# Optimization experiments

Hardware: AMD Instinct MI355X
Metric: run time of the kernel (lower is better)

Reference implementation:

```python
import jax, jax.numpy as jnp
from jax import lax
import numpy as np

INPUT_SIZE = 128
T = 64
B = 8192
HIDDENS = [32, 16, 8]
FUTURE = 1


def _lstm_layer(x, w_ih, w_hh, b_ih, b_hh):
    """PyTorch-semantics single-layer LSTM, batch_first, zero init state.
    x: [B,T,D]; w_ih: [4H,D]; w_hh: [4H,H]; b_ih,b_hh: [4H]. Gate order i,f,g,o.
    Returns all hidden states [B,T,H]."""
    Bsz = x.shape[0]
    H = w_hh.shape[1]
    # Precompute input contribution for all timesteps in one big GEMM.
    xg = jnp.einsum('btd,gd->btg', x, w_ih) + b_ih + b_hh  # [B,T,4H]
    xg_t = jnp.swapaxes(xg, 0, 1)  # [T,B,4H]

    def step(carry, xt):
        h, c = carry
        gates = xt + h @ w_hh.T  # [B,4H]
        i, f, g, o = jnp.split(gates, 4, axis=-1)
        i = jax.nn.sigmoid(i)
        f = jax.nn.sigmoid(f)
        g = jnp.tanh(g)
        o = jax.nn.sigmoid(o)
        c = f * c + i * g
        h = o * jnp.tanh(c)
        return (h, c), h

    init = (jnp.zeros((Bsz, H), x.dtype), jnp.zeros((Bsz, H), x.dtype))
    _, hs = lax.scan(step, init, xg_t)  # hs: [T,B,H]
    return jnp.swapaxes(hs, 0, 1)


def setup_inputs() -> dict:
    key = jax.random.key(0)
    ks = jax.random.split(key, 16)
    s = 0.1

    def rn(k, shape):
        return jax.random.normal(k, shape, dtype=jnp.float32) * s

    inp = {
        'x': jax.random.normal(ks[0], (B, T, INPUT_SIZE), dtype=jnp.float32),
        'w_ih1': rn(ks[1], (4 * 32, INPUT_SIZE)),
        'w_hh1': rn(ks[2], (4 * 32, 32)),
        'b_ih1': rn(ks[3], (4 * 32,)),
        'b_hh1': rn(ks[4], (4 * 32,)),
        'w_ih2': rn(ks[5], (4 * 16, 32)),
        'w_hh2': rn(ks[6], (4 * 16, 16)),
        'b_ih2': rn(ks[7], (4 * 16,)),
        'b_hh2': rn(ks[8], (4 * 16,)),
        'w_ih3': rn(ks[9], (4 * 8, 16)),
        'w_hh3': rn(ks[10], (4 * 8, 8)),
        'b_ih3': rn(ks[11], (4 * 8,)),
        'b_hh3': rn(ks[12], (4 * 8,)),
        'fc_w': rn(ks[13], (FUTURE, 8)),
        'fc_b': rn(ks[14], (FUTURE,)),
    }
    return inp


def reference(x, w_ih1, w_hh1, b_ih1, b_hh1, w_ih2, w_hh2, b_ih2, b_hh2,
              w_ih3, w_hh3, b_ih3, b_hh3, fc_w, fc_b):
    h = _lstm_layer(x, w_ih1, w_hh1, b_ih1, b_hh1)   # [B,T,32]
    h = _lstm_layer(h, w_ih2, w_hh2, b_ih2, b_hh2)   # [B,T,16]
    h = _lstm_layer(h, w_ih3, w_hh3, b_ih3, b_hh3)   # [B,T,8]
    return h[:, -1, :] @ fc_w.T + fc_b               # [B, FUTURE]
```

## Files before the change

### kernel.cpp

```cpp
#include <hip/hip_runtime.h>
#include <cstddef>
#include <type_traits>


typedef _Float16 h8_t  __attribute__((ext_vector_type(8)));
typedef __fp16   p2_t  __attribute__((ext_vector_type(2)));
typedef float    f4_t  __attribute__((ext_vector_type(4)));

#define T_LEN 64
#define D_IN  128

__device__ __forceinline__ float rcp_(float x) { return __builtin_amdgcn_rcpf(x); }

__device__ __forceinline__ float cell_(float vi, float vf, float vg, float vo,
                                       float& c) {
    float eni = __expf(-vi);
    float enf = __expf(-vf);
    float eno = __expf(-vo);
    float e2g = __expf(2.0f * vg);
    float igg = (e2g - 1.0f) * rcp_((1.0f + eni) * (e2g + 1.0f));
    c = rcp_(1.0f + enf) * c + igg;
    float t2 = fminf(fmaxf(2.0f * c, -30.0f), 30.0f);
    float e2c = __expf(t2);
    return (e2c - 1.0f) * rcp_((1.0f + eno) * (e2c + 1.0f));
}

__device__ __forceinline__ h8_t zero8h() {
    h8_t r = { (_Float16)0.f,(_Float16)0.f,(_Float16)0.f,(_Float16)0.f,
               (_Float16)0.f,(_Float16)0.f,(_Float16)0.f,(_Float16)0.f };
    return r;
}
__device__ __forceinline__ h8_t cvt8(f4_t lo, f4_t hi) {
    union { h8_t v8; p2_t v2[4]; } u;
    u.v2[0] = __builtin_amdgcn_cvt_pkrtz(lo[0], lo[1]);
    u.v2[1] = __builtin_amdgcn_cvt_pkrtz(lo[2], lo[3]);
    u.v2[2] = __builtin_amdgcn_cvt_pkrtz(hi[0], hi[1]);
    u.v2[3] = __builtin_amdgcn_cvt_pkrtz(hi[2], hi[3]);
    return u.v8;
}
__device__ __forceinline__ h8_t load8f_h(const float* __restrict__ p) {
    f4_t lo = *(const f4_t*)p, hi = *(const f4_t*)(p + 4);
    return cvt8(lo, hi);
}

__device__ __forceinline__ void bar_lds() {
    asm volatile("s_waitcnt lgkmcnt(0)" ::: "memory");
    __builtin_amdgcn_s_barrier();
}

__global__ __launch_bounds__(256, 2)
void lstm_one(const float* __restrict__ x,
              const float* __restrict__ w_ih1, const float* __restrict__ w_hh1,
              const float* __restrict__ b_ih1, const float* __restrict__ b_hh1,
              const float* __restrict__ w_ih2, const float* __restrict__ w_hh2,
              const float* __restrict__ b_ih2, const float* __restrict__ b_hh2,
              const float* __restrict__ w_ih3, const float* __restrict__ w_hh3,
              const float* __restrict__ b_ih3, const float* __restrict__ b_hh3,
              const float* __restrict__ fc_w, const float* __restrict__ fc_b,
              float* __restrict__ out)
{
    __shared__ __align__(16) _Float16 h1s[2][16][40];
    __shared__ __align__(16) _Float16 h2s[2][16][24];
    __shared__ __align__(16) _Float16 h3s[2][16][8];
    __shared__ __align__(16) _Float16 xs[2][16 * 128];

    const int tid  = threadIdx.x;
    const int lane = tid & 63;
    const int wid  = tid >> 6;
    const int nl = lane & 15, qd = lane >> 4;
    const int n7 = nl & 7;
    const bool lo8 = (nl & 8) == 0;

    h8_t bw1[2][4], bh1[2];
    #pragma unroll
    for (int j = 0; j < 2; ++j) {
        int G = 8 * wid + n7 + 32 * ((nl >> 3) + 2 * j);
        #pragma unroll
        for (int kc = 0; kc < 4; ++kc)
            bw1[j][kc] = load8f_h(w_ih1 + G * 128 + kc * 32 + qd * 8);
        bh1[j] = load8f_h(w_hh1 + G * 32 + qd * 8);
    }
    h8_t bw2[2] = {zero8h(), zero8h()}, bh2[2] = {zero8h(), zero8h()};
    float bs2[4] = {0.f, 0.f, 0.f, 0.f};
    if (wid < 2) {
        #pragma unroll
        for (int j = 0; j < 2; ++j) {
            int G = 32 * j + 16 * (nl >> 3) + 8 * wid + n7;
            bw2[j] = load8f_h(w_ih2 + G * 32 + qd * 8);
            bh2[j] = (qd < 2) ? load8f_h(w_hh2 + G * 16 + qd * 8) : zero8h();
        }
        int u2 = 8 * wid + n7;
        #pragma unroll
        for (int g = 0; g < 4; ++g) bs2[g] = b_ih2[16 * g + u2] + b_hh2[16 * g + u2];
    }
    h8_t b3c[2] = {zero8h(), zero8h()};
    float bs3[4] = {0.f, 0.f, 0.f, 0.f};
    if (wid >= 2) {
        #pragma unroll
        for (int j = 0; j < 2; ++j) {
            int G = 16 * j + 8 * (nl >> 3) + n7;
            b3c[j] = (qd < 2) ? load8f_h(w_ih3 + G * 16 + qd * 8)
                   : (qd == 2) ? load8f_h(w_hh3 + G * 8) : zero8h();
        }
        #pragma unroll
        for (int g = 0; g < 4; ++g) bs3[g] = b_ih3[8 * g + n7] + b_hh3[8 * g + n7];
    }
    float bs1[4];
    {
        int u1 = 8 * wid + n7;
        #pragma unroll
        for (int g = 0; g < 4; ++g) bs1[g] = b_ih1[32 * g + u1] + b_hh1[32 * g + u1];
    }

    for (int i = tid; i < 2 * 16 * 40; i += 256) (&h1s[0][0][0])[i] = (_Float16)0.f;
    for (int i = tid; i < 2 * 16 * 24; i += 256) (&h2s[0][0][0])[i] = (_Float16)0.f;
    for (int i = tid; i < 2 * 16 * 8;  i += 256) (&h3s[0][0][0])[i] = (_Float16)0.f;

    float c1[2] = {0.f, 0.f};
    float c2[2] = {0.f, 0.f};
    float c3    = 0.f;

    const int b0 = blockIdx.x * 16;

    const int xrow = tid >> 4, xcc = tid & 15;
    const float* xg = x + ((size_t)(b0 + xrow) * T_LEN) * D_IN + xcc * 8;
    const int xws = (xrow * 16 + (xcc ^ (xrow & 7))) * 8;

    f4_t xa0 = *(const f4_t*)xg, xa1 = *(const f4_t*)(xg + 4);
    *(h8_t*)&xs[0][xws] = cvt8(xa0, xa1);
    xa0 = *(const f4_t*)(xg + D_IN);
    xa1 = *(const f4_t*)(xg + D_IN + 4);
    bar_lds();

    auto step = [&](auto d1c, auto d2c, auto d3c, auto pc, int t) {
        constexpr bool DO1 = decltype(d1c)::value;
        constexpr bool DO2 = decltype(d2c)::value;
        constexpr bool DO3 = decltype(d3c)::value;
        constexpr int  P   = decltype(pc)::value;

        h8_t a1p = zero8h();
        if constexpr (DO1 || DO2)
            a1p = *(const h8_t*)&h1s[1 - P][nl][qd * 8];

        if constexpr (DO1) {
            h8_t af[4];
            #pragma unroll
            for (int kc = 0; kc < 4; ++kc)
                af[kc] = *(const h8_t*)&xs[P][(nl * 16 + ((4 * kc + qd) ^ n7)) * 8];

            h8_t xcur = cvt8(xa0, xa1);
            {
                int tn = (t + 2 < T_LEN) ? (t + 2) : (T_LEN - 1);
                const float* xn = xg + (size_t)tn * D_IN;
                xa0 = *(const f4_t*)xn;
                xa1 = *(const f4_t*)(xn + 4);
            }
            *(h8_t*)&xs[1 - P][xws] = xcur;

            f4_t acc[2];
            #pragma unroll
            for (int j = 0; j < 2; ++j) {
                f4_t a_ = {0.f, 0.f, 0.f, 0.f};
                #pragma unroll
                for (int kc = 0; kc < 4; ++kc)
                    a_ = __builtin_amdgcn_mfma_f32_16x16x32_f16(af[kc], bw1[j][kc], a_, 0, 0, 0);
                a_ = __builtin_amdgcn_mfma_f32_16x16x32_f16(a1p, bh1[j], a_, 0, 0, 0);
                acc[j] = a_;
            }
            #pragma unroll
            for (int rr = 0; rr < 2; ++rr) {
                float s0 = lo8 ? acc[0][rr + 2] : acc[0][rr];
                float s1 = lo8 ? acc[1][rr + 2] : acc[1][rr];
                float x0 = __shfl_xor(s0, 8, 64);
                float x1 = __shfl_xor(s1, 8, 64);
                float vi = lo8 ? acc[0][rr] : x0;
                float vf = lo8 ? x0 : acc[0][rr + 2];
                float vg = lo8 ? acc[1][rr] : x1;
                float vo = lo8 ? x1 : acc[1][rr + 2];
                float h = cell_(vi + bs1[0], vf + bs1[1], vg + bs1[2], vo + bs1[3], c1[rr]);
                h1s[P][4 * qd + rr + (lo8 ? 0 : 2)][8 * wid + n7] = (_Float16)h;
            }
        }

        if constexpr (DO2) {
            if (wid < 2) {
                h8_t a2p = zero8h();
                if (qd < 2) a2p = *(const h8_t*)&h2s[P][nl][qd * 8];
                f4_t acc2[2];
                #pragma unroll
                for (int j = 0; j < 2; ++j) {
                    f4_t a_ = {0.f, 0.f, 0.f, 0.f};
                    a_ = __builtin_amdgcn_mfma_f32_16x16x32_f16(a1p, bw2[j], a_, 0, 0, 0);
                    a_ = __builtin_amdgcn_mfma_f32_16x16x32_f16(a2p, bh2[j], a_, 0, 0, 0);
                    acc2[j] = a_;
                }
                #pragma unroll
                for (int rr = 0; rr < 2; ++rr) {
                    float s0 = lo8 ? acc2[0][rr + 2] : acc2[0][rr];
                    float s1 = lo8 ? acc2[1][rr + 2] : acc2[1][rr];
                    float x0 = __shfl_xor(s0, 8, 64);
                    float x1 = __shfl_xor(s1, 8, 64);
                    float vi = lo8 ? acc2[0][rr] : x0;
                    float vf = lo8 ? x0 : acc2[0][rr + 2];
                    float vg = lo8 ? acc2[1][rr] : x1;
                    float vo = lo8 ? x1 : acc2[1][rr + 2];
                    float h = cell_(vi + bs2[0], vf + bs2[1], vg + bs2[2], vo + bs2[3], c2[rr]);
                    h2s[1 - P][4 * qd + rr + (lo8 ? 0 : 2)][8 * wid + n7] = (_Float16)h;
                }
            }
        }

        if constexpr (DO3) {
            if (wid >= 2) {
                h8_t a3 = zero8h();
                if (qd < 2)       a3 = *(const h8_t*)&h2s[P][nl][qd * 8];
                else if (qd == 2) a3 = *(const h8_t*)&h3s[1 - P][nl][0];
                f4_t acc3[2];
                #pragma unroll
                for (int j = 0; j < 2; ++j) {
                    f4_t a_ = {0.f, 0.f, 0.f, 0.f};
                    acc3[j] = __builtin_amdgcn_mfma_f32_16x16x32_f16(a3, b3c[j], a_, 0, 0, 0);
                }
                auto l3c = [&](auto rpc) {
                    constexpr int rp = decltype(rpc)::value;
                    float eLo = acc3[0][rp],     oLo = acc3[1][rp];
                    float eHi = acc3[0][rp + 2], oHi = acc3[1][rp + 2];
                    float se = lo8 ? eHi : eLo; float xe = __shfl_xor(se, 8, 64);
                    float so = lo8 ? oHi : oLo; float xo = __shfl_xor(so, 8, 64);
                    float vi = lo8 ? eLo : xe;
                    float vf = lo8 ? xe  : eHi;
                    float vg = lo8 ? oLo : xo;
                    float vo = lo8 ? xo  : oHi;
                    float h = cell_(vi + bs3[0], vf + bs3[1], vg + bs3[2], vo + bs3[3], c3);
                    h3s[P][4 * qd + rp + (lo8 ? 0 : 2)][n7] = (_Float16)h;
                };
                if (wid == 2) l3c(std::integral_constant<int, 0>{});
                else          l3c(std::integral_constant<int, 1>{});
            }
        }

        bar_lds();
    };

    using TT = std::integral_constant<bool, true>;
    using FF = std::integral_constant<bool, false>;
    using P0 = std::integral_constant<int, 0>;
    using P1 = std::integral_constant<int, 1>;

    step(TT{}, FF{}, FF{}, P0{}, 0);
    step(TT{}, TT{}, FF{}, P1{}, 1);
    for (int tb = 1; tb < 32; ++tb) {
        step(TT{}, TT{}, TT{}, P0{}, 2 * tb);
        step(TT{}, TT{}, TT{}, P1{}, 2 * tb + 1);
    }
    step(FF{}, TT{}, TT{}, P0{}, 64);
    step(FF{}, FF{}, TT{}, P1{}, 65);

    if (tid < 16) {
        float a = fc_b[0];
        #pragma unroll
        for (int u = 0; u < 8; ++u)
            a += fc_w[u] * (float)h3s[1][tid][u];
        out[b0 + tid] = a;
    }
}

extern "C" void kernel_launch(void* const* d_in, const int* in_sizes, int n_in,
                              void* d_out, int out_size, void* d_ws, size_t ws_size,
                              hipStream_t stream) {
    (void)in_sizes; (void)n_in; (void)out_size; (void)d_ws; (void)ws_size;
    const float* x     = (const float*)d_in[0];
    const float* w_ih1 = (const float*)d_in[1];
    const float* w_hh1 = (const float*)d_in[2];
    const float* b_ih1 = (const float*)d_in[3];
    const float* b_hh1 = (const float*)d_in[4];
    const float* w_ih2 = (const float*)d_in[5];
    const float* w_hh2 = (const float*)d_in[6];
    const float* b_ih2 = (const float*)d_in[7];
    const float* b_hh2 = (const float*)d_in[8];
    const float* w_ih3 = (const float*)d_in[9];
    const float* w_hh3 = (const float*)d_in[10];
    const float* b_ih3 = (const float*)d_in[11];
    const float* b_hh3 = (const float*)d_in[12];
    const float* fc_w  = (const float*)d_in[13];
    const float* fc_b  = (const float*)d_in[14];

    dim3 grid(512), block(256);
    hipLaunchKernelGGL(lstm_one, grid, block, 0, stream,
                       x, w_ih1, w_hh1, b_ih1, b_hh1,
                       w_ih2, w_hh2, b_ih2, b_hh2,
                       w_ih3, w_hh3, b_ih3, b_hh3,
                       fc_w, fc_b, (float*)d_out);
}
```

Measured before the change: 391.0 us.

## Load x directly into MFMA fragment registers and split MFMA accumulation chains

Drops the shared-memory staging buffer for x. Each lane now loads its own 32 fp32 input values per timestep straight into registers in MFMA A-fragment layout, prefetching one step ahead instead of two. This removes the LDS write and swizzled reads for x, though each wave now loads the full 16x128 tile redundantly instead of sharing one load across the block. The dependent MFMA chains are also split into independent partial accumulators that are summed with vector adds, which shortens the dependency latency on the serial recurrence path.

```diff
diff --git a/kernel.cpp b/kernel.cpp
--- a/kernel.cpp
+++ b/kernel.cpp
@@ -62,7 +62,6 @@
     __shared__ __align__(16) _Float16 h1s[2][16][40];
     __shared__ __align__(16) _Float16 h2s[2][16][24];
     __shared__ __align__(16) _Float16 h3s[2][16][8];
-    __shared__ __align__(16) _Float16 xs[2][16 * 128];
 
     const int tid  = threadIdx.x;
     const int lane = tid & 63;
@@ -122,14 +121,13 @@
 
     const int b0 = blockIdx.x * 16;
 
-    const int xrow = tid >> 4, xcc = tid & 15;
-    const float* xg = x + ((size_t)(b0 + xrow) * T_LEN) * D_IN + xcc * 8;
-    const int xws = (xrow * 16 + (xcc ^ (xrow & 7))) * 8;
-
-    f4_t xa0 = *(const f4_t*)xg, xa1 = *(const f4_t*)(xg + 4);
-    *(h8_t*)&xs[0][xws] = cvt8(xa0, xa1);
-    xa0 = *(const f4_t*)(xg + D_IN);
-    xa1 = *(const f4_t*)(xg + D_IN + 4);
+    const float* xgl = x + ((size_t)(b0 + nl) * T_LEN) * D_IN + qd * 8;
+    f4_t xr[8];
+    #pragma unroll
+    for (int kc = 0; kc < 4; ++kc) {
+        xr[2 * kc]     = *(const f4_t*)(xgl + kc * 32);
+        xr[2 * kc + 1] = *(const f4_t*)(xgl + kc * 32 + 4);
+    }
     bar_lds();
 
     auto step = [&](auto d1c, auto d2c, auto d3c, auto pc, int t) {
@@ -145,27 +143,27 @@
         if constexpr (DO1) {
             h8_t af[4];
             #pragma unroll
-            for (int kc = 0; kc < 4; ++kc)
-                af[kc] = *(const h8_t*)&xs[P][(nl * 16 + ((4 * kc + qd) ^ n7)) * 8];
-
-            h8_t xcur = cvt8(xa0, xa1);
+            for (int kc = 0; kc < 4; ++kc) af[kc] = cvt8(xr[2 * kc], xr[2 * kc + 1]);
             {
-                int tn = (t + 2 < T_LEN) ? (t + 2) : (T_LEN - 1);
-                const float* xn = xg + (size_t)tn * D_IN;
-                xa0 = *(const f4_t*)xn;
-                xa1 = *(const f4_t*)(xn + 4);
-            }
-            *(h8_t*)&xs[1 - P][xws] = xcur;
+                int tn = (t + 1 < T_LEN) ? (t + 1) : t;
+                const float* xn = xgl + (size_t)tn * D_IN;
+                #pragma unroll
+                for (int kc = 0; kc < 4; ++kc) {
+                    xr[2 * kc]     = *(const f4_t*)(xn + kc * 32);
+                    xr[2 * kc + 1] = *(const f4_t*)(xn + kc * 32 + 4);
+                }
+            }
 
             f4_t acc[2];
             #pragma unroll
             for (int j = 0; j < 2; ++j) {
-                f4_t a_ = {0.f, 0.f, 0.f, 0.f};
-                #pragma unroll
-                for (int kc = 0; kc < 4; ++kc)
-                    a_ = __builtin_amdgcn_mfma_f32_16x16x32_f16(af[kc], bw1[j][kc], a_, 0, 0, 0);
-                a_ = __builtin_amdgcn_mfma_f32_16x16x32_f16(a1p, bh1[j], a_, 0, 0, 0);
-                acc[j] = a_;
+                f4_t z = {0.f, 0.f, 0.f, 0.f};
+                f4_t ax = __builtin_amdgcn_mfma_f32_16x16x32_f16(af[0], bw1[j][0], z, 0, 0, 0);
+                ax = __builtin_amdgcn_mfma_f32_16x16x32_f16(af[1], bw1[j][1], ax, 0, 0, 0);
+                f4_t ay = __builtin_amdgcn_mfma_f32_16x16x32_f16(af[2], bw1[j][2], z, 0, 0, 0);
+                ay = __builtin_amdgcn_mfma_f32_16x16x32_f16(af[3], bw1[j][3], ay, 0, 0, 0);
+                f4_t ah = __builtin_amdgcn_mfma_f32_16x16x32_f16(a1p, bh1[j], z, 0, 0, 0);
+                acc[j] = (ax + ay) + ah;
             }
             #pragma unroll
             for (int rr = 0; rr < 2; ++rr) {
@@ -189,10 +187,10 @@
                 f4_t acc2[2];
                 #pragma unroll
                 for (int j = 0; j < 2; ++j) {
-                    f4_t a_ = {0.f, 0.f, 0.f, 0.f};
-                    a_ = __builtin_amdgcn_mfma_f32_16x16x32_f16(a1p, bw2[j], a_, 0, 0, 0);
-                    a_ = __builtin_amdgcn_mfma_f32_16x16x32_f16(a2p, bh2[j], a_, 0, 0, 0);
-                    acc2[j] = a_;
+                    f4_t z = {0.f, 0.f, 0.f, 0.f};
+                    f4_t m1 = __builtin_amdgcn_mfma_f32_16x16x32_f16(a1p, bw2[j], z, 0, 0, 0);
+                    f4_t m2 = __builtin_amdgcn_mfma_f32_16x16x32_f16(a2p, bh2[j], z, 0, 0, 0);
+                    acc2[j] = m1 + m2;
                 }
                 #pragma unroll
                 for (int rr = 0; rr < 2; ++rr) {
@@ -218,8 +216,8 @@
                 f4_t acc3[2];
                 #pragma unroll
                 for (int j = 0; j < 2; ++j) {
-                    f4_t a_ = {0.f, 0.f, 0.f, 0.f};
-                    acc3[j] = __builtin_amdgcn_mfma_f32_16x16x32_f16(a3, b3c[j], a_, 0, 0, 0);
+                    f4_t z = {0.f, 0.f, 0.f, 0.f};
+                    acc3[j] = __builtin_amdgcn_mfma_f32_16x16x32_f16(a3, b3c[j], z, 0, 0, 0);
                 }
                 auto l3c = [&](auto rpc) {
                     constexpr int rp = decltype(rpc)::value;
```

Result: slower. 418.0 us (+6.9%).

## Make each wave own four batch rows independently, removing block barriers per step

Applied to the files above, without the earlier changes.

Reassigns work so each wavefront processes its own 4 batch rows through all three LSTM layers, instead of four waves cooperating on 16 rows with per-step block barriers. The per-step s_barrier is removed because all cross-step state is wave-private, and layer-2/3 and recurrent layer-1 weights move to a shared LDS pool. The cost is that MFMA tiles now use only 4 of 16 rows, so matrix work per useful row grows about fourfold. Each wave also runs every layer's cell math, and the extra weight registers and LDS reads add pressure.

```diff
diff --git a/kernel.cpp b/kernel.cpp
--- a/kernel.cpp
+++ b/kernel.cpp
@@ -9,6 +9,7 @@
 
 #define T_LEN 64
 #define D_IN  128
+#define XS_STR 132
 
 __device__ __forceinline__ float rcp_(float x) { return __builtin_amdgcn_rcpf(x); }
 
@@ -43,11 +44,6 @@
     return cvt8(lo, hi);
 }
 
-__device__ __forceinline__ void bar_lds() {
-    asm volatile("s_waitcnt lgkmcnt(0)" ::: "memory");
-    __builtin_amdgcn_s_barrier();
-}
-
 __global__ __launch_bounds__(256, 2)
 void lstm_one(const float* __restrict__ x,
               const float* __restrict__ w_ih1, const float* __restrict__ w_hh1,
@@ -59,78 +55,100 @@
               const float* __restrict__ fc_w, const float* __restrict__ fc_b,
               float* __restrict__ out)
 {
-    __shared__ __align__(16) _Float16 h1s[2][16][40];
-    __shared__ __align__(16) _Float16 h2s[2][16][24];
-    __shared__ __align__(16) _Float16 h3s[2][16][8];
-    __shared__ __align__(16) _Float16 xs[2][16 * 128];
+    __shared__ __align__(16) _Float16 h1s[4][2][4][40];
+    __shared__ __align__(16) _Float16 h2s[4][2][4][24];
+    __shared__ __align__(16) _Float16 h3s[4][2][4][8];
+    __shared__ __align__(16) _Float16 xs [4][2][4][XS_STR];
+    __shared__ __align__(16) _Float16 wpool[18][64][8];
+    __shared__ __align__(16) _Float16 zpad[8];
 
     const int tid  = threadIdx.x;
     const int lane = tid & 63;
     const int wid  = tid >> 6;
     const int nl = lane & 15, qd = lane >> 4;
     const int n7 = nl & 7;
-    const bool lo8 = (nl & 8) == 0;
-
-    h8_t bw1[2][4], bh1[2];
+    const int hi8 = (nl >> 3) & 1;
+    const bool lo8 = hi8 == 0;
+    const int row4 = nl & 3;
+    const bool q1 = (qd & 1) != 0, q2 = (qd & 2) != 0;
+
+    auto RS = [&](f4_t a) -> float {
+        float t01 = q1 ? a[1] : a[0];
+        float t23 = q1 ? a[3] : a[2];
+        return q2 ? t23 : t01;
+    };
+
+    h8_t bw1[4][2][4];
+    #pragma unroll
+    for (int w = 0; w < 4; ++w)
     #pragma unroll
     for (int j = 0; j < 2; ++j) {
-        int G = 8 * wid + n7 + 32 * ((nl >> 3) + 2 * j);
+        int G = 8 * w + n7 + 32 * (hi8 + 2 * j);
         #pragma unroll
         for (int kc = 0; kc < 4; ++kc)
-            bw1[j][kc] = load8f_h(w_ih1 + G * 128 + kc * 32 + qd * 8);
-        bh1[j] = load8f_h(w_hh1 + G * 32 + qd * 8);
-    }
-    h8_t bw2[2] = {zero8h(), zero8h()}, bh2[2] = {zero8h(), zero8h()};
-    float bs2[4] = {0.f, 0.f, 0.f, 0.f};
-    if (wid < 2) {
+            bw1[w][j][kc] = load8f_h(w_ih1 + G * 128 + kc * 32 + qd * 8);
+    }
+    float bs1[2][4];
+    #pragma unroll
+    for (int s = 0; s < 2; ++s) {
+        int u = n7 + 8 * s + 16 * hi8;
+        #pragma unroll
+        for (int g = 0; g < 4; ++g) bs1[s][g] = b_ih1[32 * g + u] + b_hh1[32 * g + u];
+    }
+    float bs2[4];
+    {
+        int u = n7 + 8 * hi8;
+        #pragma unroll
+        for (int g = 0; g < 4; ++g) bs2[g] = b_ih2[16 * g + u] + b_hh2[16 * g + u];
+    }
+    float bs3[4];
+    #pragma unroll
+    for (int g = 0; g < 4; ++g) bs3[g] = b_ih3[8 * g + n7] + b_hh3[8 * g + n7];
+
+    if (wid == 0) {
+        #pragma unroll
+        for (int a = 0; a < 2; ++a)
         #pragma unroll
         for (int j = 0; j < 2; ++j) {
-            int G = 32 * j + 16 * (nl >> 3) + 8 * wid + n7;
-            bw2[j] = load8f_h(w_ih2 + G * 32 + qd * 8);
-            bh2[j] = (qd < 2) ? load8f_h(w_hh2 + G * 16 + qd * 8) : zero8h();
-        }
-        int u2 = 8 * wid + n7;
-        #pragma unroll
-        for (int g = 0; g < 4; ++g) bs2[g] = b_ih2[16 * g + u2] + b_hh2[16 * g + u2];
-    }
-    h8_t b3c[2] = {zero8h(), zero8h()};
-    float bs3[4] = {0.f, 0.f, 0.f, 0.f};
-    if (wid >= 2) {
+            int G2 = 8 * a + n7 + 16 * (hi8 + 2 * j);
+            *(h8_t*)&wpool[2 * a + j][lane][0] = load8f_h(w_ih2 + G2 * 32 + qd * 8);
+            h8_t v = (qd < 2) ? load8f_h(w_hh2 + G2 * 16 + qd * 8) : zero8h();
+            *(h8_t*)&wpool[4 + 2 * a + j][lane][0] = v;
+        }
         #pragma unroll
         for (int j = 0; j < 2; ++j) {
-            int G = 16 * j + 8 * (nl >> 3) + n7;
-            b3c[j] = (qd < 2) ? load8f_h(w_ih3 + G * 16 + qd * 8)
-                   : (qd == 2) ? load8f_h(w_hh3 + G * 8) : zero8h();
-        }
-        #pragma unroll
-        for (int g = 0; g < 4; ++g) bs3[g] = b_ih3[8 * g + n7] + b_hh3[8 * g + n7];
-    }
-    float bs1[4];
-    {
-        int u1 = 8 * wid + n7;
-        #pragma unroll
-        for (int g = 0; g < 4; ++g) bs1[g] = b_ih1[32 * g + u1] + b_hh1[32 * g + u1];
-    }
-
-    for (int i = tid; i < 2 * 16 * 40; i += 256) (&h1s[0][0][0])[i] = (_Float16)0.f;
-    for (int i = tid; i < 2 * 16 * 24; i += 256) (&h2s[0][0][0])[i] = (_Float16)0.f;
-    for (int i = tid; i < 2 * 16 * 8;  i += 256) (&h3s[0][0][0])[i] = (_Float16)0.f;
-
-    float c1[2] = {0.f, 0.f};
-    float c2[2] = {0.f, 0.f};
-    float c3    = 0.f;
-
-    const int b0 = blockIdx.x * 16;
-
-    const int xrow = tid >> 4, xcc = tid & 15;
-    const float* xg = x + ((size_t)(b0 + xrow) * T_LEN) * D_IN + xcc * 8;
-    const int xws = (xrow * 16 + (xcc ^ (xrow & 7))) * 8;
-
-    f4_t xa0 = *(const f4_t*)xg, xa1 = *(const f4_t*)(xg + 4);
-    *(h8_t*)&xs[0][xws] = cvt8(xa0, xa1);
-    xa0 = *(const f4_t*)(xg + D_IN);
-    xa1 = *(const f4_t*)(xg + D_IN + 4);
-    bar_lds();
+            int G3 = n7 + 8 * (hi8 + 2 * j);
+            h8_t v = (qd < 2) ? load8f_h(w_ih3 + G3 * 16 + qd * 8)
+                   : (qd == 2) ? load8f_h(w_hh3 + G3 * 8) : zero8h();
+            *(h8_t*)&wpool[8 + j][lane][0] = v;
+        }
+        #pragma unroll
+        for (int w = 0; w < 4; ++w)
+        #pragma unroll
+        for (int j = 0; j < 2; ++j) {
+            int G = 8 * w + n7 + 32 * (hi8 + 2 * j);
+            *(h8_t*)&wpool[10 + 2 * w + j][lane][0] = load8f_h(w_hh1 + G * 32 + qd * 8);
+        }
+    }
+    for (int i = tid; i < 4 * 2 * 4 * 40; i += 256) (&h1s[0][0][0][0])[i] = (_Float16)0.f;
+    for (int i = tid; i < 4 * 2 * 4 * 24; i += 256) (&h2s[0][0][0][0])[i] = (_Float16)0.f;
+    for (int i = tid; i < 4 * 2 * 4 * 8;  i += 256) (&h3s[0][0][0][0])[i] = (_Float16)0.f;
+    if (tid < 8) zpad[tid] = (_Float16)0.f;
+
+    const int b0r = (blockIdx.x * 4 + wid) * 4;
+    const float* xrow = x + (size_t)(b0r + row4) * T_LEN * D_IN;
+    const int chunk = (nl >> 2) + 4 * qd;
+    const float* xst = xrow + chunk * 8;
+
+    f4_t xa0 = *(const f4_t*)xst, xa1 = *(const f4_t*)(xst + 4);
+    *(h8_t*)&xs[wid][0][row4][chunk * 8] = cvt8(xa0, xa1);
+    xa0 = *(const f4_t*)(xst + D_IN);
+    xa1 = *(const f4_t*)(xst + D_IN + 4);
+
+    __syncthreads();
+
+    float c1s[2] = {0.f, 0.f};
+    float c2v = 0.f, c3v = 0.f;
 
     auto step = [&](auto d1c, auto d2c, auto d3c, auto pc, int t) {
         constexpr bool DO1 = decltype(d1c)::value;
@@ -138,108 +156,104 @@
         constexpr bool DO3 = decltype(d3c)::value;
         constexpr int  P   = decltype(pc)::value;
 
-        h8_t a1p = zero8h();
+        h8_t a1p = zero8h(), a23 = zero8h();
         if constexpr (DO1 || DO2)
-            a1p = *(const h8_t*)&h1s[1 - P][nl][qd * 8];
+            a1p = *(const h8_t*)&h1s[wid][1 - P][row4][qd * 8];
+        if constexpr (DO2 || DO3) {
+            const _Float16* ap = (qd < 2) ? &h2s[wid][P][row4][qd * 8]
+                              : (qd == 2) ? &h3s[wid][1 - P][row4][0]
+                                          : &zpad[0];
+            a23 = *(const h8_t*)ap;
+        }
 
         if constexpr (DO1) {
             h8_t af[4];
             #pragma unroll
             for (int kc = 0; kc < 4; ++kc)
-                af[kc] = *(const h8_t*)&xs[P][(nl * 16 + ((4 * kc + qd) ^ n7)) * 8];
+                af[kc] = *(const h8_t*)&xs[wid][P][row4][kc * 32 + qd * 8];
 
             h8_t xcur = cvt8(xa0, xa1);
             {
                 int tn = (t + 2 < T_LEN) ? (t + 2) : (T_LEN - 1);
-                const float* xn = xg + (size_t)tn * D_IN;
-                xa0 = *(const f4_t*)xn;
-                xa1 = *(const f4_t*)(xn + 4);
+                xa0 = *(const f4_t*)(xst + (size_t)tn * D_IN);
+                xa1 = *(const f4_t*)(xst + (size_t)tn * D_IN + 4);
             }
-            *(h8_t*)&xs[1 - P][xws] = xcur;
-
-            f4_t acc[2];
+            *(h8_t*)&xs[wid][1 - P][row4][chunk * 8] = xcur;
+
+            #pragma unroll
+            for (int s = 0; s < 2; ++s) {
+                f4_t A[2][2];
+                #pragma unroll
+                for (int tw = 0; tw < 2; ++tw) {
+                    int w = s + 2 * tw;
+                    #pragma unroll
+                    for (int j = 0; j < 2; ++j) {
+                        h8_t wh = *(const h8_t*)&wpool[10 + 2 * w + j][lane][0];
+                        f4_t a_ = {0.f, 0.f, 0.f, 0.f};
+                        #pragma unroll
+                        for (int kc = 0; kc < 4; ++kc)
+                            a_ = __builtin_amdgcn_mfma_f32_16x16x32_f16(af[kc], bw1[w][j][kc], a_, 0, 0, 0);
+                        a_ = __builtin_amdgcn_mfma_f32_16x16x32_f16(a1p, wh, a_, 0, 0, 0);
+                        A[tw][j] = a_;
+                    }
+                }
+                float ra0 = RS(A[0][0]), rb0 = RS(A[1][0]);
+                float own0 = lo8 ? ra0 : rb0;
+                float rec0 = __shfl_xor(lo8 ? rb0 : ra0, 8, 64);
+                float ra1 = RS(A[0][1]), rb1 = RS(A[1][1]);
+                float own1 = lo8 ? ra1 : rb1;
+                float rec1 = __shfl_xor(lo8 ? rb1 : ra1, 8, 64);
+                float vi = lo8 ? own0 : rec0;
+                float vf = lo8 ? rec0 : own0;
+                float vg = lo8 ? own1 : rec1;
+                float vo = lo8 ? rec1 : own1;
+                float h = cell_(vi + bs1[s][0], vf + bs1[s][1],
+                                vg + bs1[s][2], vo + bs1[s][3], c1s[s]);
+                h1s[wid][P][qd][n7 + 8 * s + 16 * hi8] = (_Float16)h;
+            }
+        }
+
+        if constexpr (DO2) {
+            f4_t A[2][2];
+            #pragma unroll
+            for (int a = 0; a < 2; ++a)
             #pragma unroll
             for (int j = 0; j < 2; ++j) {
+                h8_t wb = *(const h8_t*)&wpool[2 * a + j][lane][0];
+                h8_t wh = *(const h8_t*)&wpool[4 + 2 * a + j][lane][0];
                 f4_t a_ = {0.f, 0.f, 0.f, 0.f};
-                #pragma unroll
-                for (int kc = 0; kc < 4; ++kc)
-                    a_ = __builtin_amdgcn_mfma_f32_16x16x32_f16(af[kc], bw1[j][kc], a_, 0, 0, 0);
-                a_ = __builtin_amdgcn_mfma_f32_16x16x32_f16(a1p, bh1[j], a_, 0, 0, 0);
-                acc[j] = a_;
+                a_ = __builtin_amdgcn_mfma_f32_16x16x32_f16(a1p, wb, a_, 0, 0, 0);
+                a_ = __builtin_amdgcn_mfma_f32_16x16x32_f16(a23, wh, a_, 0, 0, 0);
+                A[a][j] = a_;
             }
-            #pragma unroll
-            for (int rr = 0; rr < 2; ++rr) {
-                float s0 = lo8 ? acc[0][rr + 2] : acc[0][rr];
-                float s1 = lo8 ? acc[1][rr + 2] : acc[1][rr];
-                float x0 = __shfl_xor(s0, 8, 64);
-                float x1 = __shfl_xor(s1, 8, 64);
-                float vi = lo8 ? acc[0][rr] : x0;
-                float vf = lo8 ? x0 : acc[0][rr + 2];
-                float vg = lo8 ? acc[1][rr] : x1;
-                float vo = lo8 ? x1 : acc[1][rr + 2];
-                float h = cell_(vi + bs1[0], vf + bs1[1], vg + bs1[2], vo + bs1[3], c1[rr]);
-                h1s[P][4 * qd + rr + (lo8 ? 0 : 2)][8 * wid + n7] = (_Float16)h;
+            float ra0 = RS(A[0][0]), rb0 = RS(A[1][0]);
+            float own0 = lo8 ? ra0 : rb0;
+            float rec0 = __shfl_xor(lo8 ? rb0 : ra0, 8, 64);
+            float ra1 = RS(A[0][1]), rb1 = RS(A[1][1]);
+            float own1 = lo8 ? ra1 : rb1;
+            float rec1 = __shfl_xor(lo8 ? rb1 : ra1, 8, 64);
+            float vi = lo8 ? own0 : rec0;
+            float vf = lo8 ? rec0 : own0;
+            float vg = lo8 ? own1 : rec1;
+            float vo = lo8 ? rec1 : own1;
+            float h = cell_(vi + bs2[0], vf + bs2[1], vg + bs2[2], vo + bs2[3], c2v);
+            h2s[wid][1 - P][qd][n7 + 8 * hi8] = (_Float16)h;
+        }
+
+        if constexpr (DO3) {
+            f4_t A3[2];
+            #pragma unroll
+            for (int j = 0; j < 2; ++j) {
+                h8_t wb = *(const h8_t*)&wpool[8 + j][lane][0];
+                f4_t z = {0.f, 0.f, 0.f, 0.f};
+                A3[j] = __builtin_amdgcn_mfma_f32_16x16x32_f16(a23, wb, z, 0, 0, 0);
             }
-        }
-
-        if constexpr (DO2) {
-            if (wid < 2) {
-                h8_t a2p = zero8h();
-                if (qd < 2) a2p = *(const h8_t*)&h2s[P][nl][qd * 8];
-                f4_t acc2[2];
-                #pragma unroll
-                for (int j = 0; j < 2; ++j) {
-                    f4_t a_ = {0.f, 0.f, 0.f, 0.f};
-                    a_ = __builtin_amdgcn_mfma_f32_16x16x32_f16(a1p, bw2[j], a_, 0, 0, 0);
-                    a_ = __builtin_amdgcn_mfma_f32_16x16x32_f16(a2p, bh2[j], a_, 0, 0, 0);
-                    acc2[j] = a_;
-                }
-                #pragma unroll
-                for (int rr = 0; rr < 2; ++rr) {
-                    float s0 = lo8 ? acc2[0][rr + 2] : acc2[0][rr];
-                    float s1 = lo8 ? acc2[1][rr + 2] : acc2[1][rr];
-                    float x0 = __shfl_xor(s0, 8, 64);
-                    float x1 = __shfl_xor(s1, 8, 64);
-                    float vi = lo8 ? acc2[0][rr] : x0;
-                    float vf = lo8 ? x0 : acc2[0][rr + 2];
-                    float vg = lo8 ? acc2[1][rr] : x1;
-                    float vo = lo8 ? x1 : acc2[1][rr + 2];
-                    float h = cell_(vi + bs2[0], vf + bs2[1], vg + bs2[2], vo + bs2[3], c2[rr]);
-                    h2s[1 - P][4 * qd + rr + (lo8 ? 0 : 2)][8 * wid + n7] = (_Float16)h;
-                }
-            }
-        }
-
-        if constexpr (DO3) {
-            if (wid >= 2) {
-                h8_t a3 = zero8h();
-                if (qd < 2)       a3 = *(const h8_t*)&h2s[P][nl][qd * 8];
-                else if (qd == 2) a3 = *(const h8_t*)&h3s[1 - P][nl][0];
-                f4_t acc3[2];
-                #pragma unroll
-                for (int j = 0; j < 2; ++j) {
-                    f4_t a_ = {0.f, 0.f, 0.f, 0.f};
-                    acc3[j] = __builtin_amdgcn_mfma_f32_16x16x32_f16(a3, b3c[j], a_, 0, 0, 0);
-                }
-                auto l3c = [&](auto rpc) {
-                    constexpr int rp = decltype(rpc)::value;
-                    float eLo = acc3[0][rp],     oLo = acc3[1][rp];
-                    float eHi = acc3[0][rp + 2], oHi = acc3[1][rp + 2];
-                    float se = lo8 ? eHi : eLo; float xe = __shfl_xor(se, 8, 64);
-                    float so = lo8 ? oHi : oLo; float xo = __shfl_xor(so, 8, 64);
-                    float vi = lo8 ? eLo : xe;
-                    float vf = lo8 ? xe  : eHi;
-                    float vg = lo8 ? oLo : xo;
-                    float vo = lo8 ? xo  : oHi;
-                    float h = cell_(vi + bs3[0], vf + bs3[1], vg + bs3[2], vo + bs3[3], c3);
-                    h3s[P][4 * qd + rp + (lo8 ? 0 : 2)][n7] = (_Float16)h;
-                };
-                if (wid == 2) l3c(std::integral_constant<int, 0>{});
-                else          l3c(std::integral_constant<int, 1>{});
-            }
-        }
-
-        bar_lds();
+            float r0 = RS(A3[0]), r1 = RS(A3[1]);
+            float x0 = __shfl_xor(r0, 8, 64);
+            float x1 = __shfl_xor(r1, 8, 64);
+            float h = cell_(r0 + bs3[0], x0 + bs3[1], r1 + bs3[2], x1 + bs3[3], c3v);
+            if (lo8) h3s[wid][P][qd][n7] = (_Float16)h;
+        }
     };
 
     using TT = std::integral_constant<bool, true>;
@@ -256,12 +270,12 @@
     step(FF{}, TT{}, TT{}, P0{}, 64);
     step(FF{}, FF{}, TT{}, P1{}, 65);
 
-    if (tid < 16) {
+    if (lane < 4) {
         float a = fc_b[0];
         #pragma unroll
         for (int u = 0; u < 8; ++u)
-            a += fc_w[u] * (float)h3s[1][tid][u];
-        out[b0 + tid] = a;
+            a += fc_w[u] * (float)h3s[wid][1][lane][u];
+        out[b0r + lane] = a;
     }
 }
 
```

After: 550.0 us. 40.6% more time.
